# Performance work log

Measured on AMD Instinct MI355X. Metric: run time of the kernel, lower is better.

## Reference

```python
import jax, jax.numpy as jnp
import numpy as np

N_ENTRIES = 4_194_304   # total CSR entries (gene observations)
H, W = 256, 256
N_PIXELS = H * W
N_GENES = 30000
FEATURE_DIM = 64


def setup_inputs() -> dict:
    key = jax.random.key(0)
    k1, k2, k3, k4 = jax.random.split(key, 4)
    # gene id per CSR entry
    indices = jax.random.randint(k1, (N_ENTRIES,), 0, N_GENES, dtype=jnp.int64)
    # counts per entry (positive floats)
    cnts = jax.random.uniform(k2, (N_ENTRIES,), dtype=jnp.float32) * 10.0
    # CSR row pointers over pixels: sorted, starting at 0, ending at N_ENTRIES
    indptr = jnp.sort(jax.random.randint(k3, (N_PIXELS + 1,), 0, N_ENTRIES + 1, dtype=jnp.int64))
    indptr = indptr.at[0].set(0).at[-1].set(N_ENTRIES)
    # params: gamma init zeros, tokens variance_scaling(1.0,'fan_in','normal',out_axis=0)
    gamma = jnp.zeros((N_GENES,), jnp.float32)
    tokens = jax.random.normal(k4, (N_GENES, FEATURE_DIM), dtype=jnp.float32) * (1.0 / np.sqrt(FEATURE_DIM))
    return {"indices": indices, "cnts": cnts, "indptr": indptr, "gamma": gamma, "tokens": tokens}


def reference(indices, cnts, indptr, gamma, tokens):
    # SGStem with rescale=True, normalize=False (module defaults)
    n_entries = indices.shape[0]
    n_pixels = indptr.shape[0] - 1  # == H*W
    # mask padding entries beyond indptr[-1]
    valid = jnp.arange(n_entries) < indptr[-1]
    c = jnp.where(valid, cnts, 0.0)
    # rescale counts by per-gene exp(gamma)
    c = c * jnp.exp(gamma[indices])
    # CSR -> segment ids per entry
    rpt = jnp.diff(indptr)
    segms = jnp.repeat(jnp.arange(n_pixels), rpt, total_repeat_length=n_entries)
    # gather token embeddings, scale, scatter-add into pixel bins
    embeddings = tokens[indices] * c[:, None]  # (n_entries, feature_dim)
    embedding_sum = jax.ops.segment_sum(embeddings, segms, num_segments=n_pixels)
    return embedding_sum.reshape(H, W, tokens.shape[-1])
```

## Files before the change

### kernel.cpp

```cpp
#include <hip/hip_runtime.h>
#include <hip/hip_bf16.h>

#define FDIM 64
#define N_PIXELS 65536
#define N_GENES 30000
#define WAVES_PER_BLOCK 4
#define PIX_PER_WAVE 8

__device__ __forceinline__ unsigned short f32_to_bf16_rne(float f) {
    unsigned int u = __float_as_uint(f);
    u = (u + 0x7FFFu + ((u >> 16) & 1u)) >> 16;
    return (unsigned short)u;
}

__global__ __launch_bounds__(256) void convert_tokens(
    const float4* __restrict__ tokens4,
    ushort4* __restrict__ tok_bf)
{
    const int i = blockIdx.x * blockDim.x + threadIdx.x;
    const float4 t = tokens4[i];
    ushort4 o;
    o.x = f32_to_bf16_rne(t.x);
    o.y = f32_to_bf16_rne(t.y);
    o.z = f32_to_bf16_rne(t.z);
    o.w = f32_to_bf16_rne(t.w);
    tok_bf[i] = o;
}

__global__ __launch_bounds__(WAVES_PER_BLOCK * 64) void sgstem_main(
    const int* __restrict__ indices,
    const float* __restrict__ cnts,
    const int* __restrict__ indptr,
    const float* __restrict__ gamma,
    const uint4* __restrict__ tok_bf,
    float4* __restrict__ out4)
{
    __shared__ int2 meta[WAVES_PER_BLOCK][64];

    const int lane = threadIdx.x & 63;
    const int wave = threadIdx.x >> 6;
    const int g    = lane >> 3;
    const int fl   = lane & 7;
    const int wgid = blockIdx.x * WAVES_PER_BLOCK + wave;
    const int p0   = wgid * PIX_PER_WAVE;

    for (int pixel = p0; pixel < p0 + PIX_PER_WAVE; ++pixel) {
        const int start = indptr[pixel];
        const int end   = indptr[pixel + 1];

        float a0 = 0.f, a1 = 0.f, a2 = 0.f, a3 = 0.f;
        float a4 = 0.f, a5 = 0.f, a6 = 0.f, a7 = 0.f;

        for (int base = start; base < end; base += 64) {
            const int e = base + lane;
            int   idx   = 0;
            float scale = 0.0f;
            if (e < end) {
                idx   = indices[e];
                scale = cnts[e] * __expf(gamma[idx]);
            }
            int2 mt;
            mt.x = idx;
            mt.y = __float_as_int(scale);
            meta[wave][lane] = mt;

            const int m = end - base;
            if (m >= 64) {
                #pragma unroll 8
                for (int j = 0; j < 8; ++j) {
                    const int2 mm = meta[wave][j * 8 + g];
                    const float s = __int_as_float(mm.y);
                    const uint4 t = tok_bf[mm.x * 8 + fl];
                    a0 = fmaf(__uint_as_float(t.x << 16), s, a0);
                    a1 = fmaf(__uint_as_float(t.x & 0xFFFF0000u), s, a1);
                    a2 = fmaf(__uint_as_float(t.y << 16), s, a2);
                    a3 = fmaf(__uint_as_float(t.y & 0xFFFF0000u), s, a3);
                    a4 = fmaf(__uint_as_float(t.z << 16), s, a4);
                    a5 = fmaf(__uint_as_float(t.z & 0xFFFF0000u), s, a5);
                    a6 = fmaf(__uint_as_float(t.w << 16), s, a6);
                    a7 = fmaf(__uint_as_float(t.w & 0xFFFF0000u), s, a7);
                }
            } else {
                const int niter = (m + 7) >> 3;
                for (int j = 0; j < niter; ++j) {
                    const int2 mm = meta[wave][j * 8 + g];
                    const float s = __int_as_float(mm.y);
                    const uint4 t = tok_bf[mm.x * 8 + fl];
                    a0 = fmaf(__uint_as_float(t.x << 16), s, a0);
                    a1 = fmaf(__uint_as_float(t.x & 0xFFFF0000u), s, a1);
                    a2 = fmaf(__uint_as_float(t.y << 16), s, a2);
                    a3 = fmaf(__uint_as_float(t.y & 0xFFFF0000u), s, a3);
                    a4 = fmaf(__uint_as_float(t.z << 16), s, a4);
                    a5 = fmaf(__uint_as_float(t.z & 0xFFFF0000u), s, a5);
                    a6 = fmaf(__uint_as_float(t.w << 16), s, a6);
                    a7 = fmaf(__uint_as_float(t.w & 0xFFFF0000u), s, a7);
                }
            }
        }

        #pragma unroll
        for (int mask = 8; mask <= 32; mask <<= 1) {
            a0 += __shfl_xor(a0, mask);
            a1 += __shfl_xor(a1, mask);
            a2 += __shfl_xor(a2, mask);
            a3 += __shfl_xor(a3, mask);
            a4 += __shfl_xor(a4, mask);
            a5 += __shfl_xor(a5, mask);
            a6 += __shfl_xor(a6, mask);
            a7 += __shfl_xor(a7, mask);
        }

        if (g == 0) {
            float4 lo = make_float4(a0, a1, a2, a3);
            float4 hi = make_float4(a4, a5, a6, a7);
            out4[pixel * 16 + fl * 2]     = lo;
            out4[pixel * 16 + fl * 2 + 1] = hi;
        }
    }
}

extern "C" void kernel_launch(void* const* d_in, const int* in_sizes, int n_in,
                              void* d_out, int out_size, void* d_ws, size_t ws_size,
                              hipStream_t stream) {
    const int*    indices = (const int*)d_in[0];
    const float*  cnts    = (const float*)d_in[1];
    const int*    indptr  = (const int*)d_in[2];
    const float*  gamma   = (const float*)d_in[3];
    const float4* tokens4 = (const float4*)d_in[4];
    float4*       out4    = (float4*)d_out;

    ushort4* tok_bf = (ushort4*)d_ws;

    convert_tokens<<<1875, 256, 0, stream>>>(tokens4, tok_bf);

    const int nblocks = N_PIXELS / (WAVES_PER_BLOCK * PIX_PER_WAVE);
    sgstem_main<<<nblocks, WAVES_PER_BLOCK * 64, 0, stream>>>(
        indices, cnts, indptr, gamma, (const uint4*)tok_bf, out4);
}
```

Baseline: 165.3 us.

## Balance work by splitting CSR entries evenly across waves with atomic boundary merges

Waves now each take a fixed, equal slice of CSR entries instead of a fixed count of pixels. Each wave binary-searches indptr to find its first pixel, writes pixels that lie wholly inside its slice directly, and uses float atomics for pixels split across slices. This targets load imbalance from the uneven, random per-pixel entry counts. In exchange it adds an output memset, a binary search per wave and boundary atomics, which make the summation order for split pixels nondeterministic.

```diff
diff --git a/kernel.cpp b/kernel.cpp
--- a/kernel.cpp
+++ b/kernel.cpp
@@ -3,9 +3,11 @@
 
 #define FDIM 64
 #define N_PIXELS 65536
+#define N_ENTRIES 4194304
 #define N_GENES 30000
 #define WAVES_PER_BLOCK 4
-#define PIX_PER_WAVE 8
+#define N_WAVES 8192
+#define EPW (N_ENTRIES / N_WAVES)
 
 __device__ __forceinline__ unsigned short f32_to_bf16_rne(float f) {
     unsigned int u = __float_as_uint(f);
@@ -33,7 +35,7 @@
     const int* __restrict__ indptr,
     const float* __restrict__ gamma,
     const uint4* __restrict__ tok_bf,
-    float4* __restrict__ out4)
+    float* __restrict__ out)
 {
     __shared__ int2 meta[WAVES_PER_BLOCK][64];
 
@@ -41,81 +43,93 @@
     const int wave = threadIdx.x >> 6;
     const int g    = lane >> 3;
     const int fl   = lane & 7;
-    const int wgid = blockIdx.x * WAVES_PER_BLOCK + wave;
-    const int p0   = wgid * PIX_PER_WAVE;
 
-    for (int pixel = p0; pixel < p0 + PIX_PER_WAVE; ++pixel) {
-        const int start = indptr[pixel];
-        const int end   = indptr[pixel + 1];
+    const int wid = __builtin_amdgcn_readfirstlane(
+        blockIdx.x * WAVES_PER_BLOCK + wave);
+    const int e0 = wid * EPW;
+    const int e1 = e0 + EPW;
 
-        float a0 = 0.f, a1 = 0.f, a2 = 0.f, a3 = 0.f;
-        float a4 = 0.f, a5 = 0.f, a6 = 0.f, a7 = 0.f;
+    int lo = 0, hi = N_PIXELS;
+    while (lo < hi) {
+        const int mid = (lo + hi + 1) >> 1;
+        if (indptr[mid] <= e0) lo = mid; else hi = mid - 1;
+    }
+    int p = lo;
 
-        for (int base = start; base < end; base += 64) {
-            const int e = base + lane;
-            int   idx   = 0;
-            float scale = 0.0f;
-            if (e < end) {
-                idx   = indices[e];
-                scale = cnts[e] * __expf(gamma[idx]);
-            }
-            int2 mt;
-            mt.x = idx;
-            mt.y = __float_as_int(scale);
-            meta[wave][lane] = mt;
+    while (p < N_PIXELS) {
+        const int ps = indptr[p];
+        if (ps >= e1) break;
+        const int pe = indptr[p + 1];
+        const int s = max(ps, e0);
+        const int t = min(pe, e1);
 
-            const int m = end - base;
-            if (m >= 64) {
-                #pragma unroll 8
-                for (int j = 0; j < 8; ++j) {
-                    const int2 mm = meta[wave][j * 8 + g];
-                    const float s = __int_as_float(mm.y);
-                    const uint4 t = tok_bf[mm.x * 8 + fl];
-                    a0 = fmaf(__uint_as_float(t.x << 16), s, a0);
-                    a1 = fmaf(__uint_as_float(t.x & 0xFFFF0000u), s, a1);
-                    a2 = fmaf(__uint_as_float(t.y << 16), s, a2);
-                    a3 = fmaf(__uint_as_float(t.y & 0xFFFF0000u), s, a3);
-                    a4 = fmaf(__uint_as_float(t.z << 16), s, a4);
-                    a5 = fmaf(__uint_as_float(t.z & 0xFFFF0000u), s, a5);
-                    a6 = fmaf(__uint_as_float(t.w << 16), s, a6);
-                    a7 = fmaf(__uint_as_float(t.w & 0xFFFF0000u), s, a7);
+        if (t > s) {
+            float a0 = 0.f, a1 = 0.f, a2 = 0.f, a3 = 0.f;
+            float a4 = 0.f, a5 = 0.f, a6 = 0.f, a7 = 0.f;
+
+            for (int base = s; base < t; base += 64) {
+                const int e = base + lane;
+                int   idx   = 0;
+                float scale = 0.0f;
+                if (e < t) {
+                    idx   = indices[e];
+                    scale = cnts[e] * __expf(gamma[idx]);
                 }
-            } else {
-                const int niter = (m + 7) >> 3;
+                int2 mt;
+                mt.x = idx;
+                mt.y = __float_as_int(scale);
+                meta[wave][lane] = mt;
+
+                const int m = t - base;
+                const int niter = (m >= 64) ? 8 : ((m + 7) >> 3);
+                #pragma unroll 4
                 for (int j = 0; j < niter; ++j) {
                     const int2 mm = meta[wave][j * 8 + g];
-                    const float s = __int_as_float(mm.y);
-                    const uint4 t = tok_bf[mm.x * 8 + fl];
-                    a0 = fmaf(__uint_as_float(t.x << 16), s, a0);
-                    a1 = fmaf(__uint_as_float(t.x & 0xFFFF0000u), s, a1);
-                    a2 = fmaf(__uint_as_float(t.y << 16), s, a2);
-                    a3 = fmaf(__uint_as_float(t.y & 0xFFFF0000u), s, a3);
-                    a4 = fmaf(__uint_as_float(t.z << 16), s, a4);
-                    a5 = fmaf(__uint_as_float(t.z & 0xFFFF0000u), s, a5);
-                    a6 = fmaf(__uint_as_float(t.w << 16), s, a6);
-                    a7 = fmaf(__uint_as_float(t.w & 0xFFFF0000u), s, a7);
+                    const float sc = __int_as_float(mm.y);
+                    const uint4 tk = tok_bf[mm.x * 8 + fl];
+                    a0 = fmaf(__uint_as_float(tk.x << 16), sc, a0);
+                    a1 = fmaf(__uint_as_float(tk.x & 0xFFFF0000u), sc, a1);
+                    a2 = fmaf(__uint_as_float(tk.y << 16), sc, a2);
+                    a3 = fmaf(__uint_as_float(tk.y & 0xFFFF0000u), sc, a3);
+                    a4 = fmaf(__uint_as_float(tk.z << 16), sc, a4);
+                    a5 = fmaf(__uint_as_float(tk.z & 0xFFFF0000u), sc, a5);
+                    a6 = fmaf(__uint_as_float(tk.w << 16), sc, a6);
+                    a7 = fmaf(__uint_as_float(tk.w & 0xFFFF0000u), sc, a7);
+                }
+            }
+
+            #pragma unroll
+            for (int mask = 8; mask <= 32; mask <<= 1) {
+                a0 += __shfl_xor(a0, mask);
+                a1 += __shfl_xor(a1, mask);
+                a2 += __shfl_xor(a2, mask);
+                a3 += __shfl_xor(a3, mask);
+                a4 += __shfl_xor(a4, mask);
+                a5 += __shfl_xor(a5, mask);
+                a6 += __shfl_xor(a6, mask);
+                a7 += __shfl_xor(a7, mask);
+            }
+
+            if (g == 0) {
+                const bool interior = (ps >= e0) && (pe <= e1);
+                if (interior) {
+                    float4* o4 = (float4*)(out + p * FDIM);
+                    o4[fl * 2]     = make_float4(a0, a1, a2, a3);
+                    o4[fl * 2 + 1] = make_float4(a4, a5, a6, a7);
+                } else {
+                    float* o = out + p * FDIM + fl * 8;
+                    atomicAdd(o + 0, a0);
+                    atomicAdd(o + 1, a1);
+                    atomicAdd(o + 2, a2);
+                    atomicAdd(o + 3, a3);
+                    atomicAdd(o + 4, a4);
+                    atomicAdd(o + 5, a5);
+                    atomicAdd(o + 6, a6);
+                    atomicAdd(o + 7, a7);
                 }
             }
         }
-
-        #pragma unroll
-        for (int mask = 8; mask <= 32; mask <<= 1) {
-            a0 += __shfl_xor(a0, mask);
-            a1 += __shfl_xor(a1, mask);
-            a2 += __shfl_xor(a2, mask);
-            a3 += __shfl_xor(a3, mask);
-            a4 += __shfl_xor(a4, mask);
-            a5 += __shfl_xor(a5, mask);
-            a6 += __shfl_xor(a6, mask);
-            a7 += __shfl_xor(a7, mask);
-        }
-
-        if (g == 0) {
-            float4 lo = make_float4(a0, a1, a2, a3);
-            float4 hi = make_float4(a4, a5, a6, a7);
-            out4[pixel * 16 + fl * 2]     = lo;
-            out4[pixel * 16 + fl * 2 + 1] = hi;
-        }
+        ++p;
     }
 }
 
@@ -127,13 +141,14 @@
     const int*    indptr  = (const int*)d_in[2];
     const float*  gamma   = (const float*)d_in[3];
     const float4* tokens4 = (const float4*)d_in[4];
-    float4*       out4    = (float4*)d_out;
+    float*        out     = (float*)d_out;
 
     ushort4* tok_bf = (ushort4*)d_ws;
 
+    hipMemsetAsync(d_out, 0, (size_t)N_PIXELS * FDIM * sizeof(float), stream);
+
     convert_tokens<<<1875, 256, 0, stream>>>(tokens4, tok_bf);
 
-    const int nblocks = N_PIXELS / (WAVES_PER_BLOCK * PIX_PER_WAVE);
-    sgstem_main<<<nblocks, WAVES_PER_BLOCK * 64, 0, stream>>>(
-        indices, cnts, indptr, gamma, (const uint4*)tok_bf, out4);
+    sgstem_main<<<N_WAVES / WAVES_PER_BLOCK, WAVES_PER_BLOCK * 64, 0, stream>>>(
+        indices, cnts, indptr, gamma, (const uint4*)tok_bf, out);
 }
```

After: 162.3 us. About the same (-1.8%).
